# Performance work log

Measured on AMD Instinct MI355X. Metric: run time of the kernel, lower is better.

## Reference

```python
import jax, jax.numpy as jnp
import numpy as np

B, ARITY = 4096, 6
EMB = 100
NF = 200
FC = 1200
N_ROLES, N_VALUES = 5000, 50000
BN_EPS = 1e-5


def setup_inputs() -> dict:
    key = jax.random.key(0)
    ks = jax.random.split(key, 12)
    bound = float(np.sqrt(1.0 / EMB))
    x = jax.random.randint(ks[0], (B, 2 * ARITY), 0, 5000, dtype=jnp.int64)
    emb_roles = jax.random.uniform(ks[1], (N_ROLES, EMB), jnp.float32, -bound, bound)
    emb_values = jax.random.uniform(ks[2], (N_VALUES, EMB), jnp.float32, -bound, bound)
    conv_w = 0.1 * jax.random.normal(ks[3], (NF, 2 * EMB), jnp.float32)  # conv (1,2E) kernel == linear
    conv_b = jnp.zeros((NF,), jnp.float32)
    bn_gamma = jnp.ones((NF,), jnp.float32)
    bn_beta = jnp.zeros((NF,), jnp.float32)
    gW = jax.random.normal(ks[4], (FC, 2 * NF), jnp.float32) * float(np.sqrt(2.0 / (FC + 2 * NF)))
    gb = jnp.zeros((FC,), jnp.float32)
    fW = jax.random.normal(ks[5], (1, FC), jnp.float32) * float(np.sqrt(2.0 / (1 + FC)))
    fb = jnp.zeros((1,), jnp.float32)
    return dict(x=x, emb_roles=emb_roles, emb_values=emb_values, conv_w=conv_w,
                conv_b=conv_b, bn_gamma=bn_gamma, bn_beta=bn_beta,
                gW=gW, gb=gb, fW=fW, fb=fb)


def reference(x, emb_roles, emb_values, conv_w, conv_b, bn_gamma, bn_beta, gW, gb, fW, fb):
    arity = x.shape[1] // 2
    roles = emb_roles[x[:, 0::2]]    # [B, A, E]
    values = emb_values[x[:, 1::2]]  # [B, A, E]
    cat = jnp.concatenate([roles, values], axis=-1)  # [B, A, 2E]
    # conv1 with kernel (1, 2E) == per-row linear 2E -> NF
    m = jnp.einsum('bae,fe->baf', cat, conv_w) + conv_b  # [B, A, NF]
    # BatchNorm2d (training mode: batch statistics over B and A per channel)
    mu = m.mean(axis=(0, 1))
    var = m.var(axis=(0, 1))
    m = (m - mu) * jax.lax.rsqrt(var + BN_EPS) * bn_gamma + bn_beta
    m_rel = jax.nn.relu(m)  # [B, A, NF]
    # all role-value pairs: first tiles the sequence, second repeats each row
    first = jnp.tile(m_rel, (1, arity, 1))           # [B, A*A, NF]
    second = jnp.repeat(m_rel, arity, axis=1)        # [B, A*A, NF]
    pairs = jnp.concatenate([first, second], axis=-1)  # [B, A*A, 2NF]
    g = jax.nn.relu(jnp.einsum('bpf,of->bpo', pairs, gW) + gb)  # [B, A*A, FC]
    min_val = g.min(axis=1)  # [B, FC]
    score = min_val @ fW.T + fb  # [B, 1]
    return score
```

## Files before the change

kernel.cpp:

```cpp
#include <hip/hip_runtime.h>
#include <hip/hip_bf16.h>
#include <hip/hip_fp16.h>

#define B_    4096
#define ARITY 6
#define EMB   100
#define NF    200
#define FC    1200
#define NROWS (B_*ARITY)
#define NPAD  2432
#define BN_EPS 1e-5f
#define KP    224
#define SENT  32768.0f
#define NTW   (NPAD/4/16)

typedef _Float16 half8 __attribute__((ext_vector_type(8)));
typedef float f32x4 __attribute__((ext_vector_type(4)));

#define MRAW_OFF 0
#define WH_OFF   2457600
#define WT_OFF   2729984
#define STAT_OFF 2780160

__device__ __forceinline__ void gload16(const void* g, void* l) {
    __builtin_amdgcn_global_load_lds(
        (const __attribute__((address_space(1))) void*)g,
        (__attribute__((address_space(3))) void*)l, 16, 0, 0);
}

__device__ __forceinline__ float4 ld4(const float* rr, const float* vr, int e) {
    if (e < EMB)        return *(const float4*)&rr[e];
    else if (e < 2*EMB) return *(const float4*)&vr[e - EMB];
    float4 z = {0.f,0.f,0.f,0.f}; return z;
}

#define K0_W1 (224*28)
#define K0_W2 (K0_W1 + NPAD*28)
#define K0_W3 (K0_W2 + B_)
#define K0_TOT (K0_W3 + 6400)
__launch_bounds__(256)
__global__ void k0_prep(const float* __restrict__ cw, const float* __restrict__ gW,
                        const float* __restrict__ fb,
                        _Float16* __restrict__ wT,
                        _Float16* __restrict__ W_h, float* __restrict__ out,
                        float* __restrict__ gshad)
{
    int id = blockIdx.x * 256 + threadIdx.x;
    if (id < K0_W1) {
        int f = id / 28, s = id - f*28;
        int ks = s >> 2, ls = s & 3, key = (f >> 1) & 3;
        int off = ks*14336 + f*32 + ((ls ^ key)*8);
        half8 h, l;
        #pragma unroll
        for (int j = 0; j < 8; ++j) {
            int k = s*8 + j;
            float v = (f < NF && k < NF) ? cw[f*NF + k] : 0.f;
            _Float16 hi = (_Float16)v;
            h[j] = hi; l[j] = (_Float16)(v - (float)hi);
        }
        *(half8*)&wT[off] = h;
        *(half8*)&wT[off + 7168] = l;
    } else if (id < K0_W2) {
        int id2 = id - K0_W1;
        int n = id2 / 28, s = id2 - n*28;
        int o = n >> 1, hf = n & 1;
        int off = (n >> 4)*3584 + (s >> 2)*512 + (n & 15)*32 + (s & 3)*8;
        half8 h;
        #pragma unroll
        for (int j = 0; j < 8; ++j) {
            int k = s*8 + j;
            float v = 0.f;
            if (k < NF && n < 2*FC) v = gW[(size_t)o*400 + hf*200 + k];
            if (k == NF) v = SENT;
            h[j] = (_Float16)v;
        }
        *(half8*)&W_h[off] = h;
    } else if (id < K0_W3) {
        out[id - K0_W2] = fb[0];
    } else if (id < K0_TOT) {
        gshad[id - K0_W3] = 0.f;
    }
}

__launch_bounds__(256)
__global__ void k1_mfma(const int* __restrict__ x,
                        const float* __restrict__ er,
                        const float* __restrict__ ev,
                        const _Float16* __restrict__ wT,
                        const float* __restrict__ cb,
                        _Float16* __restrict__ m_raw,
                        float* __restrict__ gshad)
{
    __shared__ __align__(16) char smem[59200];
    float* s_sum = (float*)(smem + 57344);
    float* s_sq  = (float*)(smem + 58144);
    int*   s_ri  = (int*)(smem + 58944);
    int*   s_vi  = (int*)(smem + 59072);

    const int t = threadIdx.x, lane = t & 63, wave = t >> 6;
    const int wm = wave >> 1, wn = wave & 1;
    const int R0 = blockIdx.x * 32;
    const int q = lane >> 4, cx = lane & 15;
    const int rdsw = (q ^ ((cx >> 1) & 3)) * 8;

    if (t < 32) {
        int R = R0 + t, b = R / ARITY, a = R - b * ARITY;
        bool is64 = ((x[1] | x[3] | x[5] | x[7]) == 0);
        int base = b * (2*ARITY) + 2*a;
        s_ri[t] = is64 ? x[2*base]     : x[base];
        s_vi[t] = is64 ? x[2*base + 2] : x[base + 1];
    }
    if (t < NF) { s_sum[t] = 0.f; s_sq[t] = 0.f; }
    __syncthreads();

    {
        _Float16* s_ahi = (_Float16*)smem;
        _Float16* s_alo = s_ahi + 7168;
        for (int c = t; c < 896; c += 256) {
            int row = c / 28, s = c - row*28;
            int key = (row >> 1) & 3;
            int col = (s >> 2)*32 + ((s & 3) ^ key)*8;
            const float* rr = er + (size_t)s_ri[row] * EMB;
            const float* vr = ev + (size_t)s_vi[row] * EMB;
            int e0 = s*8;
            float4 v0 = ld4(rr, vr, e0);
            float4 v1 = ld4(rr, vr, e0 + 4);
            half8 hi, lo;
            hi[0]=(_Float16)v0.x; lo[0]=(_Float16)(v0.x-(float)hi[0]);
            hi[1]=(_Float16)v0.y; lo[1]=(_Float16)(v0.y-(float)hi[1]);
            hi[2]=(_Float16)v0.z; lo[2]=(_Float16)(v0.z-(float)hi[2]);
            hi[3]=(_Float16)v0.w; lo[3]=(_Float16)(v0.w-(float)hi[3]);
            hi[4]=(_Float16)v1.x; lo[4]=(_Float16)(v1.x-(float)hi[4]);
            hi[5]=(_Float16)v1.y; lo[5]=(_Float16)(v1.y-(float)hi[5]);
            hi[6]=(_Float16)v1.z; lo[6]=(_Float16)(v1.z-(float)hi[6]);
            hi[7]=(_Float16)v1.w; lo[7]=(_Float16)(v1.w-(float)hi[7]);
            *(half8*)&s_ahi[row*KP + col] = hi;
            *(half8*)&s_alo[row*KP + col] = lo;
        }
    }
    __syncthreads();

    f32x4 ah[7], al[7];
    {
        const _Float16* s_ahi = (const _Float16*)smem;
        const _Float16* s_alo = s_ahi + 7168;
        int arow = wm*16 + cx;
        #pragma unroll
        for (int ks = 0; ks < 7; ++ks) {
            ah[ks] = *(const f32x4*)&s_ahi[arow*KP + ks*32 + rdsw];
            al[ks] = *(const f32x4*)&s_alo[arow*KP + ks*32 + rdsw];
            asm volatile("" : "+v"(ah[ks]), "+v"(al[ks]));
        }
    }
    __syncthreads();

    #define STAGE_W(KS_, BUF_) do {                                          \
        const char* _src = (const char*)wT + (size_t)(KS_) * 28672;          \
        char* _dst = smem + (BUF_) * 28672;                                  \
        _Pragma("unroll")                                                    \
        for (int _i = 0; _i < 7; ++_i) {                                     \
            int _j = wave + 4*_i;                                            \
            gload16(_src + (size_t)(_j*64 + lane)*16, _dst + _j*1024);       \
        }                                                                    \
    } while (0)

    STAGE_W(0, 0);
    STAGE_W(1, 1);

    f32x4 acc[7];
    #pragma unroll
    for (int nf = 0; nf < 7; ++nf) acc[nf] = (f32x4){0.f,0.f,0.f,0.f};

    for (int ks = 0; ks < 7; ++ks) {
        if (ks < 6) asm volatile("s_waitcnt vmcnt(7)" ::: "memory");
        else        asm volatile("s_waitcnt vmcnt(0)" ::: "memory");
        __builtin_amdgcn_s_barrier();
        __builtin_amdgcn_sched_barrier(0);

        const _Float16* wb = (const _Float16*)(smem + (ks & 1) * 28672);
        #pragma unroll
        for (int nf = 0; nf < 7; ++nf) {
            int rb = (wn*112 + nf*16 + cx)*32 + rdsw;
            half8 bh = *(const half8*)&wb[rb];
            half8 bl = *(const half8*)&wb[7168 + rb];
            acc[nf] = __builtin_amdgcn_mfma_f32_16x16x32_f16(
                __builtin_bit_cast(half8, ah[ks]), bh, acc[nf], 0,0,0);
            acc[nf] = __builtin_amdgcn_mfma_f32_16x16x32_f16(
                __builtin_bit_cast(half8, ah[ks]), bl, acc[nf], 0,0,0);
            acc[nf] = __builtin_amdgcn_mfma_f32_16x16x32_f16(
                __builtin_bit_cast(half8, al[ks]), bh, acc[nf], 0,0,0);
        }
        asm volatile("s_waitcnt lgkmcnt(0)" ::: "memory");
        __builtin_amdgcn_sched_barrier(0);
        __builtin_amdgcn_s_barrier();
        __builtin_amdgcn_sched_barrier(0);
        if (ks + 2 < 7) STAGE_W(ks + 2, ks & 1);
    }

    #pragma unroll
    for (int nf = 0; nf < 7; ++nf) {
        int f = wn*112 + nf*16 + cx;
        bool valid = (f < NF);
        float bias = valid ? cb[f] : 0.f;
        float ps = 0.f, pq = 0.f;
        #pragma unroll
        for (int reg = 0; reg < 4; ++reg) {
            float vv = acc[nf][reg] + bias;
            if (valid) {
                int R = R0 + wm*16 + q*4 + reg;
                m_raw[(size_t)R*NF + f] = (_Float16)vv;
                ps += vv; pq += vv*vv;
            }
        }
        ps += __shfl_xor(ps, 16); ps += __shfl_xor(ps, 32);
        pq += __shfl_xor(pq, 16); pq += __shfl_xor(pq, 32);
        if (valid && q == 0) { atomicAdd(&s_sum[f], ps); atomicAdd(&s_sq[f], pq); }
    }
    __syncthreads();
    if (t < NF) {
        float* g = gshad + (blockIdx.x & 15) * 400;
        atomicAdd(&g[t], s_sum[t]);
        atomicAdd(&g[t + 200], s_sq[t]);
    }
}

__launch_bounds__(256, 2)
__global__ void k3_mfma(const _Float16* __restrict__ m_raw,
                        const float* __restrict__ gshad,
                        const float* __restrict__ gamma,
                        const float* __restrict__ beta,
                        const _Float16* __restrict__ W_h,
                        const float* __restrict__ gb,
                        const float* __restrict__ fW,
                        float* __restrict__ out)
{
    __shared__ __align__(16) char smem[33024];
    float2* gbfw2 = (float2*)(smem + 21504);
    float*  scsh  = (float*)(smem + 31232);

    const int t = threadIdx.x, lane = t & 63, wave = t >> 6;
    const int q = lane >> 4, cx = lane & 15;
    const int rdsw = (q ^ ((cx >> 1) & 3)) * 8;

    if (t < 224) {
        float sc = 0.f, sh = 0.f;
        if (t < NF) {
            float s = 0.f, qq = 0.f;
            #pragma unroll
            for (int c = 0; c < 16; ++c) { s += gshad[c*400 + t]; qq += gshad[c*400 + 200 + t]; }
            float inv = 1.0f / (float)NROWS;
            float mu  = s * inv;
            float var = qq * inv - mu*mu;
            float rs  = rsqrtf(var + BN_EPS);
            sc = rs * gamma[t];
            sh = beta[t] - mu*sc;
        }
        scsh[t] = sc; scsh[224 + t] = sh;
    }
    for (int i = t; i < 1216; i += 256) {
        float g = (i < FC) ? gb[i] : 0.f;
        float f = (i < FC) ? fW[i] : 0.f;
        gbfw2[i] = make_float2(g, f);
    }
    __syncthreads();

    {
        _Float16* sa = (_Float16*)smem;
        for (int c = t; c < 1344; c += 256) {
            int row = c / 28, s = c - row*28;
            int key = (row >> 1) & 3;
            int col = (s >> 2)*32 + ((s & 3) ^ key)*8;
            half8 o;
            #pragma unroll
            for (int j = 0; j < 8; ++j) o[j] = (_Float16)0.f;
            if (s < 25) {
                int R = blockIdx.x*48 + row;
                half8 in = *(const half8*)&m_raw[(size_t)R*NF + s*8];
                #pragma unroll
                for (int j = 0; j < 8; ++j) {
                    int k = s*8 + j;
                    o[j] = (_Float16)fmaxf((float)in[j]*scsh[k] + scsh[224+k], 0.f);
                }
            }
            *(half8*)&sa[row*KP + col] = o;
        }
    }
    __syncthreads();

    f32x4 av[3][7];
    {
        const _Float16* sa = (const _Float16*)smem;
        #pragma unroll
        for (int mf = 0; mf < 3; ++mf) {
            int row = mf*16 + cx;
            #pragma unroll
            for (int ks = 0; ks < 7; ++ks)
                av[mf][ks] = *(const f32x4*)&sa[row*KP + ks*32 + rdsw];
        }
    }

    const int nbase = wave * (NPAD/4);
    const char* wsrc = (const char*)W_h + (size_t)nbase * 448;
    const int boff = cx*64 + q*16;

    #define LOADT(BV_, NT_) do {                                             \
        const char* _b = wsrc + (size_t)(NT_)*7168 + boff;                   \
        _Pragma("unroll")                                                    \
        for (int _k = 0; _k < 7; ++_k)                                       \
            BV_[_k] = *(const f32x4*)(_b + _k*1024);                         \
    } while (0)

    #define MFMAT(BV_, ACC_) do {                                            \
        _Pragma("unroll")                                                    \
        for (int _m = 0; _m < 3; ++_m) ACC_[_m] = (f32x4){0.f,0.f,0.f,0.f};  \
        _Pragma("unroll")                                                    \
        for (int _k = 0; _k < 7; ++_k) {                                     \
            _Pragma("unroll")                                                \
            for (int _m = 0; _m < 3; ++_m)                                   \
                ACC_[_m] = __builtin_amdgcn_mfma_f32_16x16x32_f16(           \
                    __builtin_bit_cast(half8, av[_m][_k]),                   \
                    __builtin_bit_cast(half8, BV_[_k]), ACC_[_m], 0, 0, 0);  \
        }                                                                    \
    } while (0)

    float preg16 = 0.f, preg48 = 0.f;

    #define EPI(ACC_, NT_) do {                                              \
        float _h0l = fminf(ACC_[0][0], ACC_[0][1]);                          \
        float _h0h = fminf(ACC_[0][2], ACC_[0][3]);                          \
        float _h1l = fminf(ACC_[1][0], ACC_[1][1]);                          \
        float _h1h = fminf(ACC_[1][2], ACC_[1][3]);                          \
        float _h2l = fminf(ACC_[2][0], ACC_[2][1]);                          \
        float _h2h = fminf(ACC_[2][2], ACC_[2][3]);                          \
        float _f0 = fminf(_h0l, _h0h);                                       \
        float _f1 = fminf(_h1l, _h1h);                                       \
        float _f2 = fminf(_h2l, _h2h);                                       \
        float _u16 = (q==0) ? _h1h : (q==1) ? _h0l : (q==2) ? _h2h : _h1l;   \
        float _u48 = (q==0) ? _h1l : (q==1) ? _h0h : (q==2) ? _h2l : _h1h;   \
        float _F16 = (q==0) ? _f0 : (q==3) ? _f2 : _f1;                      \
        float _F48 = (q<=1) ? _f2 : _f0;                                     \
        float _v16 = fminf(_F16, __shfl_xor(_u16, 16));                      \
        float _v48 = fminf(_F48, __shfl_xor(_u48, 48));                      \
        float _vp16 = _v16 + __shfl_xor(_v16, 1);                            \
        float _vp48 = _v48 + __shfl_xor(_v48, 1);                            \
        float2 _gf = gbfw2[(nbase + (NT_)*16 + cx) >> 1];                    \
        if ((cx & 1) == 0) {                                                 \
            preg16 += fmaxf(_vp16 + _gf.x, 0.f) * _gf.y;                     \
            preg48 += fmaxf(_vp48 + _gf.x, 0.f) * _gf.y;                     \
        }                                                                    \
    } while (0)

    f32x4 bv0[7], bv1[7];
    f32x4 acc0[3], acc1[3];

    LOADT(bv0, 0);
    LOADT(bv1, 1);
    MFMAT(bv0, acc0);
    for (int k = 0; k < 17; ++k) {
        int nt = 2*k + 1;
        LOADT(bv0, nt + 1); MFMAT(bv1, acc1); EPI(acc0, nt - 1);
        LOADT(bv1, nt + 2); MFMAT(bv0, acc0); EPI(acc1, nt);
    }
    LOADT(bv0, 36); MFMAT(bv1, acc1); EPI(acc0, 34);
    LOADT(bv1, 37); MFMAT(bv0, acc0); EPI(acc1, 35);
    MFMAT(bv1, acc1); EPI(acc0, 36);
    EPI(acc1, 37);

    preg16 += __shfl_xor(preg16, 1); preg16 += __shfl_xor(preg16, 2);
    preg16 += __shfl_xor(preg16, 4); preg16 += __shfl_xor(preg16, 8);
    preg48 += __shfl_xor(preg48, 1); preg48 += __shfl_xor(preg48, 2);
    preg48 += __shfl_xor(preg48, 4); preg48 += __shfl_xor(preg48, 8);
    if (cx == 0) {
        int b16 = (q==0) ? 0 : (q==1) ? 3 : (q==2) ? 4 : 7;
        int b48 = (q==0) ? 5 : (q==1) ? 6 : (q==2) ? 1 : 2;
        atomicAdd(&out[blockIdx.x*8 + b16], preg16);
        atomicAdd(&out[blockIdx.x*8 + b48], preg48);
    }
}

extern "C" void kernel_launch(void* const* d_in, const int* in_sizes, int n_in,
                              void* d_out, int out_size, void* d_ws, size_t ws_size,
                              hipStream_t stream)
{
    const int*   x   = (const int*)  d_in[0];
    const float* er  = (const float*)d_in[1];
    const float* ev  = (const float*)d_in[2];
    const float* cw  = (const float*)d_in[3];
    const float* cb  = (const float*)d_in[4];
    const float* gam = (const float*)d_in[5];
    const float* bet = (const float*)d_in[6];
    const float* gW  = (const float*)d_in[7];
    const float* gb  = (const float*)d_in[8];
    const float* fW  = (const float*)d_in[9];
    const float* fb  = (const float*)d_in[10];

    float* ws = (float*)d_ws;
    _Float16* m_raw = (_Float16*)(ws + MRAW_OFF);
    _Float16* W_h   = (_Float16*)(ws + WH_OFF);
    _Float16* wT    = (_Float16*)(ws + WT_OFF);
    float* gshad    = ws + STAT_OFF;
    float* out      = (float*)d_out;

    k0_prep<<<(K0_TOT + 255)/256, 256, 0, stream>>>(cw, gW, fb, wT, W_h, out, gshad);
    k1_mfma<<<NROWS/32, 256, 0, stream>>>(x, er, ev, wT, cb, m_raw, gshad);
    k3_mfma<<<NROWS/48, 256, 0, stream>>>(m_raw, gshad, gam, bet, W_h, gb, fW, out);
}
```

Baseline: 71.77 us.

## Single-buffer conv weight staging and triple-buffer FC weight register prefetch

Measured after the change: 66.38 us. -7.5%, faster.

```diff
diff --git a/kernel.cpp b/kernel.cpp
--- a/kernel.cpp
+++ b/kernel.cpp
@@ -91,11 +91,11 @@
                         _Float16* __restrict__ m_raw,
                         float* __restrict__ gshad)
 {
-    __shared__ __align__(16) char smem[59200];
-    float* s_sum = (float*)(smem + 57344);
-    float* s_sq  = (float*)(smem + 58144);
-    int*   s_ri  = (int*)(smem + 58944);
-    int*   s_vi  = (int*)(smem + 59072);
+    __shared__ __align__(16) char smem[30528];
+    float* s_sum = (float*)(smem + 28672);
+    float* s_sq  = (float*)(smem + 29472);
+    int*   s_ri  = (int*)(smem + 30272);
+    int*   s_vi  = (int*)(smem + 30400);
 
     const int t = threadIdx.x, lane = t & 63, wave = t >> 6;
     const int wm = wave >> 1, wn = wave & 1;
@@ -154,30 +154,24 @@
     }
     __syncthreads();
 
-    #define STAGE_W(KS_, BUF_) do {                                          \
+    #define STAGE_W(KS_) do {                                                \
         const char* _src = (const char*)wT + (size_t)(KS_) * 28672;          \
-        char* _dst = smem + (BUF_) * 28672;                                  \
         _Pragma("unroll")                                                    \
         for (int _i = 0; _i < 7; ++_i) {                                     \
             int _j = wave + 4*_i;                                            \
-            gload16(_src + (size_t)(_j*64 + lane)*16, _dst + _j*1024);       \
+            gload16(_src + (size_t)(_j*64 + lane)*16, smem + _j*1024);       \
         }                                                                    \
     } while (0)
-
-    STAGE_W(0, 0);
-    STAGE_W(1, 1);
 
     f32x4 acc[7];
     #pragma unroll
     for (int nf = 0; nf < 7; ++nf) acc[nf] = (f32x4){0.f,0.f,0.f,0.f};
 
     for (int ks = 0; ks < 7; ++ks) {
-        if (ks < 6) asm volatile("s_waitcnt vmcnt(7)" ::: "memory");
-        else        asm volatile("s_waitcnt vmcnt(0)" ::: "memory");
-        __builtin_amdgcn_s_barrier();
-        __builtin_amdgcn_sched_barrier(0);
-
-        const _Float16* wb = (const _Float16*)(smem + (ks & 1) * 28672);
+        STAGE_W(ks);
+        __syncthreads();
+
+        const _Float16* wb = (const _Float16*)smem;
         #pragma unroll
         for (int nf = 0; nf < 7; ++nf) {
             int rb = (wn*112 + nf*16 + cx)*32 + rdsw;
@@ -190,11 +184,7 @@
             acc[nf] = __builtin_amdgcn_mfma_f32_16x16x32_f16(
                 __builtin_bit_cast(half8, al[ks]), bh, acc[nf], 0,0,0);
         }
-        asm volatile("s_waitcnt lgkmcnt(0)" ::: "memory");
-        __builtin_amdgcn_sched_barrier(0);
-        __builtin_amdgcn_s_barrier();
-        __builtin_amdgcn_sched_barrier(0);
-        if (ks + 2 < 7) STAGE_W(ks + 2, ks & 1);
+        __syncthreads();
     }
 
     #pragma unroll
@@ -304,7 +294,8 @@
     const int boff = cx*64 + q*16;
 
     #define LOADT(BV_, NT_) do {                                             \
-        const char* _b = wsrc + (size_t)(NT_)*7168 + boff;                   \
+        int _nt = (NT_) > (NTW-1) ? (NTW-1) : (NT_);                         \
+        const char* _b = wsrc + (size_t)_nt*7168 + boff;                     \
         _Pragma("unroll")                                                    \
         for (int _k = 0; _k < 7; ++_k)                                       \
             BV_[_k] = *(const f32x4*)(_b + _k*1024);                         \
@@ -350,19 +341,20 @@
         }                                                                    \
     } while (0)
 
-    f32x4 bv0[7], bv1[7];
+    f32x4 bv0[7], bv1[7], bv2[7];
     f32x4 acc0[3], acc1[3];
 
-    LOADT(bv0, 0);
-    LOADT(bv1, 1);
+    LOADT(bv0, 0); LOADT(bv1, 1); LOADT(bv2, 2);
     MFMAT(bv0, acc0);
-    for (int k = 0; k < 17; ++k) {
-        int nt = 2*k + 1;
-        LOADT(bv0, nt + 1); MFMAT(bv1, acc1); EPI(acc0, nt - 1);
-        LOADT(bv1, nt + 2); MFMAT(bv0, acc0); EPI(acc1, nt);
-    }
-    LOADT(bv0, 36); MFMAT(bv1, acc1); EPI(acc0, 34);
-    LOADT(bv1, 37); MFMAT(bv0, acc0); EPI(acc1, 35);
+    for (int k = 0; k < 6; ++k) {
+        int nt = 6*k;
+        LOADT(bv0, nt + 3); MFMAT(bv1, acc1); EPI(acc0, nt + 0);
+        LOADT(bv1, nt + 4); MFMAT(bv2, acc0); EPI(acc1, nt + 1);
+        LOADT(bv2, nt + 5); MFMAT(bv0, acc1); EPI(acc0, nt + 2);
+        LOADT(bv0, nt + 6); MFMAT(bv1, acc0); EPI(acc1, nt + 3);
+        LOADT(bv1, nt + 7); MFMAT(bv2, acc1); EPI(acc0, nt + 4);
+        LOADT(bv2, nt + 8); MFMAT(bv0, acc0); EPI(acc1, nt + 5);
+    }
     MFMAT(bv1, acc1); EPI(acc0, 36);
     EPI(acc1, 37);
 
```
